# Kernel tuning notes

Measured on AMD Instinct MI355X. Metric: run time of the kernel, lower is better.

Reference implementation:

```python
import jax, jax.numpy as jnp
import numpy as np

H = 1024  # hidden_dim


def setup_inputs() -> dict:
    key = jax.random.key(0)
    ks = jax.random.split(key, 8)
    B, S = 32, 2048
    value = jax.random.normal(ks[0], (B, S, 2 * H), dtype=jnp.float32)
    query = jax.random.normal(ks[1], (B, 2 * H), dtype=jnp.float32)
    padding_mask = jnp.zeros((B, S), dtype=bool)
    pre_coverage = jax.random.uniform(ks[2], (B, S), dtype=jnp.float32)
    sc = 1.0 / np.sqrt(2 * H)
    Wv = jax.random.normal(ks[3], (2 * H, H), dtype=jnp.float32) * sc  # value_layer.weight^T
    Wq = jax.random.normal(ks[4], (2 * H, H), dtype=jnp.float32) * sc  # query_layer.weight^T
    We = jax.random.normal(ks[5], (H,), dtype=jnp.float32) * (1.0 / np.sqrt(H))  # energy_layer
    Wc = jax.random.normal(ks[6], (H,), dtype=jnp.float32)  # coverage_layer (Linear(1,H))
    return {"value": value, "query": query, "padding_mask": padding_mask,
            "pre_coverage": pre_coverage, "Wv": Wv, "Wq": Wq, "We": We, "Wc": Wc}


def reference(value, query, padding_mask, pre_coverage, Wv, Wq, We, Wc):
    # value: [B,S,2H], query: [B,2H], padding_mask: [B,S] bool, pre_coverage: [B,S]
    v = jnp.einsum('bsf,fh->bsh', value, Wv)          # projected values [B,S,H]
    q = (query @ Wq)[:, None, :]                       # [B,1,H]
    feat = q + v + pre_coverage[:, :, None] * Wc       # coverage term: Linear(1,H)
    scores = jnp.tanh(feat) @ We                       # [B,S]
    scores = jnp.where(padding_mask, -jnp.inf, scores)
    alphas = jax.nn.softmax(scores, axis=-1)           # [B,S]
    context = jnp.einsum('bs,bsh->bh', alphas, v)[:, None, :]  # [B,1,H]
    new_coverage = pre_coverage + alphas
    return context, alphas, new_coverage
```

## Files before the change

### kernel.cpp

```cpp
#include <hip/hip_runtime.h>
#include <hip/hip_bf16.h>

#define HD 1024
#define K2 2048
#define BATCH 32
#define SEQ 2048
#define M_TOT (BATCH * SEQ)

typedef __attribute__((ext_vector_type(4))) float f32x4;
typedef __attribute__((ext_vector_type(8))) short bf16x8;
typedef __attribute__((ext_vector_type(4))) unsigned short u16x4;
typedef __attribute__((ext_vector_type(8))) unsigned short u16x8;

__device__ __forceinline__ float bf2f(unsigned short u) {
    unsigned int x = ((unsigned int)u) << 16;
    return __builtin_bit_cast(float, x);
}
__device__ __forceinline__ unsigned short f2bf(float f) {
    unsigned int x = __builtin_bit_cast(unsigned int, f);
    unsigned int lsb = (x >> 16) & 1u;
    x += 0x7fffu + lsb;
    return (unsigned short)(x >> 16);
}

__device__ __forceinline__ void load_lds_16B(const void* g, void* lds) {
    __builtin_amdgcn_global_load_lds(
        (const __attribute__((address_space(1))) unsigned int*)g,
        (__attribute__((address_space(3))) unsigned int*)lds,
        16, 0, 0);
}

__global__ __launch_bounds__(256) void cvt_value_kernel(
        const float* __restrict__ A, unsigned short* __restrict__ Abf) {
    const size_t stride = (size_t)2048 * 256 * 8;
    size_t i = ((size_t)blockIdx.x * 256 + threadIdx.x) * 8;
    const size_t n = (size_t)M_TOT * K2;
    for (; i < n; i += stride) {
        f32x4 a = *reinterpret_cast<const f32x4*>(A + i);
        f32x4 b = *reinterpret_cast<const f32x4*>(A + i + 4);
        u16x8 r;
        r[0] = f2bf(a.x); r[1] = f2bf(a.y); r[2] = f2bf(a.z); r[3] = f2bf(a.w);
        r[4] = f2bf(b.x); r[5] = f2bf(b.y); r[6] = f2bf(b.z); r[7] = f2bf(b.w);
        *reinterpret_cast<u16x8*>(Abf + i) = r;
    }
}

__global__ __launch_bounds__(256) void wv_transpose_kernel(
        const float* __restrict__ Wv, unsigned short* __restrict__ WvT) {
    __shared__ float t[64][65];
    int n0 = blockIdx.x * 64;
    int k0 = blockIdx.y * 64;
    int tx = threadIdx.x & 63, ty = threadIdx.x >> 6;
#pragma unroll
    for (int rr = 0; rr < 16; ++rr) {
        int row = ty + rr * 4;
        t[row][tx] = Wv[(size_t)(k0 + row) * HD + n0 + tx];
    }
    __syncthreads();
#pragma unroll
    for (int rr = 0; rr < 16; ++rr) {
        int row = ty + rr * 4;
        WvT[(size_t)(n0 + row) * K2 + k0 + tx] = f2bf(t[tx][row]);
    }
}

__global__ __launch_bounds__(256) void qproj_kernel(
        const float* __restrict__ query, const float* __restrict__ Wq,
        float* __restrict__ qp) {
    int b = blockIdx.x >> 2;
    int h = ((blockIdx.x & 3) << 8) + threadIdx.x;
    const float* q = query + (size_t)b * K2;
    float acc = 0.f;
    for (int f = 0; f < K2; f += 4) {
        f32x4 qv = *reinterpret_cast<const f32x4*>(q + f);
        acc += qv.x * Wq[(size_t)f * HD + h];
        acc += qv.y * Wq[(size_t)(f + 1) * HD + h];
        acc += qv.z * Wq[(size_t)(f + 2) * HD + h];
        acc += qv.w * Wq[(size_t)(f + 3) * HD + h];
    }
    qp[b * HD + h] = acc;
}

#define NT 32

__device__ __forceinline__ f32x4 mfma_bf16(bf16x8 a, bf16x8 b, f32x4 c) {
    return __builtin_amdgcn_mfma_f32_16x16x32_bf16(a, b, c, 0, 0, 0);
}

template<int MB, int NB>
__device__ __forceinline__ void mfma_quad(f32x4 (&acc)[8][4],
        const bf16x8 (&af)[4][2], const bf16x8 (&bfv)[2][2]) {
#pragma unroll
    for (int f = 0; f < 4; ++f)
#pragma unroll
        for (int j = 0; j < 2; ++j) {
            acc[MB + f][NB + j] = mfma_bf16(af[f][0], bfv[j][0], acc[MB + f][NB + j]);
            acc[MB + f][NB + j] = mfma_bf16(af[f][1], bfv[j][1], acc[MB + f][NB + j]);
        }
}

__global__ __launch_bounds__(512, 2) void gemm8_kernel(
        const unsigned short* __restrict__ A,
        const unsigned short* __restrict__ BT,
        unsigned short* __restrict__ Vout) {
    __shared__ __align__(16) char lds[131072];

    const int tid  = threadIdx.x;
    const int lane = tid & 63;
    const int wave = tid >> 6;
    const int wr   = wave >> 2;
    const int wc   = wave & 3;

    int id  = blockIdx.x;
    int xcd = id & 7, sdx = id >> 3;
    int m0 = ((xcd << 5) | (sdx >> 2)) * 256;
    int n0 = (sdx & 3) * 256;

    const int off0   = wave * 1024 + lane * 16;
    const int srow   = off0 >> 7;
    const int schunk = ((off0 >> 4) & 7) ^ (srow & 7);
    const int scol   = schunk * 8;
    const unsigned short* As0 = A  + ((size_t)m0 + srow) * K2 + scol;
    const unsigned short* Bs0 = BT + ((size_t)n0 + srow) * K2 + scol;

    const int l15 = lane & 15, l4v = lane >> 4;
    const int kch0 = (l4v ^ (lane & 7)) << 4;
    const int kch1 = ((4 | l4v) ^ (lane & 7)) << 4;
    const int aRow = (wr * 128 + l15) * 128;
    const int bRow = (wc * 64 + l15) * 128;

    f32x4 acc[8][4] = {};

#define STG_A(t_, h_, p_, buf_) \
    load_lds_16B(As0 + ((size_t)((h_) * 128 + (p_) * 64)) * K2 + (t_) * 64, \
                 lds + (buf_) * 32768 + (h_) * 16384 + (p_) * 8192 + off0)
#define STG_B(t_, h_, p_, buf_) \
    load_lds_16B(Bs0 + ((size_t)((h_) * 128 + (p_) * 64)) * K2 + (t_) * 64, \
                 lds + 65536 + (buf_) * 32768 + (h_) * 16384 + (p_) * 8192 + off0)

    STG_A(0, 0, 0, 0); STG_A(0, 0, 1, 0); STG_A(0, 1, 0, 0); STG_A(0, 1, 1, 0);
    STG_B(0, 0, 0, 0); STG_B(0, 0, 1, 0); STG_B(0, 1, 0, 0); STG_B(0, 1, 1, 0);
    STG_A(1, 0, 0, 1); STG_A(1, 0, 1, 1); STG_A(1, 1, 0, 1); STG_A(1, 1, 1, 1);
    STG_B(1, 0, 0, 1); STG_B(1, 0, 1, 1); STG_B(1, 1, 0, 1); STG_B(1, 1, 1, 1);
    asm volatile("s_waitcnt vmcnt(8)" ::: "memory");
    __builtin_amdgcn_s_barrier();

    bf16x8 afr[4][2], bf0[2][2], bf1[2][2];

    for (int t = 0; t < NT; ++t) {
        const int cur = t & 1;
        const char* La = lds + cur * 32768;
        const char* Lb = lds + 65536 + cur * 32768;
        const bool pf = (t + 2 < NT);

#pragma unroll
        for (int f = 0; f < 4; ++f) {
            afr[f][0] = *(const bf16x8*)(La + aRow + f * 2048 + kch0);
            afr[f][1] = *(const bf16x8*)(La + aRow + f * 2048 + kch1);
        }
#pragma unroll
        for (int j = 0; j < 2; ++j) {
            bf0[j][0] = *(const bf16x8*)(Lb + bRow + j * 2048 + kch0);
            bf0[j][1] = *(const bf16x8*)(Lb + bRow + j * 2048 + kch1);
        }
        __builtin_amdgcn_s_barrier();
        asm volatile("s_waitcnt lgkmcnt(0)" ::: "memory");
        __builtin_amdgcn_s_setprio(1);
        mfma_quad<0, 0>(acc, afr, bf0);
        __builtin_amdgcn_s_setprio(0);
        __builtin_amdgcn_s_barrier();

#pragma unroll
        for (int j = 0; j < 2; ++j) {
            bf1[j][0] = *(const bf16x8*)(Lb + bRow + (2 + j) * 2048 + kch0);
            bf1[j][1] = *(const bf16x8*)(Lb + bRow + (2 + j) * 2048 + kch1);
        }
        if (pf) { STG_A(t + 2, 0, 0, cur); STG_A(t + 2, 1, 0, cur); }
        __builtin_amdgcn_s_barrier();
        asm volatile("s_waitcnt lgkmcnt(0)" ::: "memory");
        __builtin_amdgcn_s_setprio(1);
        mfma_quad<0, 2>(acc, afr, bf1);
        __builtin_amdgcn_s_setprio(0);
        __builtin_amdgcn_s_barrier();

#pragma unroll
        for (int f = 0; f < 4; ++f) {
            afr[f][0] = *(const bf16x8*)(La + aRow + 8192 + f * 2048 + kch0);
            afr[f][1] = *(const bf16x8*)(La + aRow + 8192 + f * 2048 + kch1);
        }
        if (pf) {
            STG_B(t + 2, 0, 0, cur); STG_B(t + 2, 0, 1, cur);
            STG_B(t + 2, 1, 0, cur); STG_B(t + 2, 1, 1, cur);
        }
        __builtin_amdgcn_s_barrier();
        asm volatile("s_waitcnt lgkmcnt(0)" ::: "memory");
        __builtin_amdgcn_s_setprio(1);
        mfma_quad<4, 2>(acc, afr, bf1);
        __builtin_amdgcn_s_setprio(0);
        __builtin_amdgcn_s_barrier();

        if (pf) { STG_A(t + 2, 0, 1, cur); STG_A(t + 2, 1, 1, cur); }
        __builtin_amdgcn_s_barrier();
        __builtin_amdgcn_s_setprio(1);
        mfma_quad<4, 0>(acc, afr, bf0);
        __builtin_amdgcn_s_setprio(0);
        if (t < NT - 1) {
            if (t < NT - 2) asm volatile("s_waitcnt vmcnt(8)" ::: "memory");
            else            asm volatile("s_waitcnt vmcnt(0)" ::: "memory");
            __builtin_amdgcn_s_barrier();
        }
    }
#undef STG_A
#undef STG_B

#pragma unroll
    for (int fi = 0; fi < 8; ++fi) {
#pragma unroll
        for (int fj = 0; fj < 4; ++fj) {
            int row = m0 + wr * 128 + fi * 16 + l4v * 4;
            int col = n0 + wc * 64 + fj * 16 + l15;
#pragma unroll
            for (int r = 0; r < 4; ++r)
                Vout[(size_t)(row + r) * HD + col] = f2bf(acc[fi][fj][r]);
        }
    }
}

#define BM 128
#define BN 128
#define BK 32
__device__ __forceinline__ void swizzle_mn(int id, int& m0, int& n0) {
    int xcd = id & 7;
    int s = id >> 3;
    int m_idx = (xcd << 6) | (s >> 3);
    int n_idx = s & 7;
    m0 = m_idx * BM;
    n0 = n_idx * BN;
}

__global__ __launch_bounds__(256) void gemm_v_kernel(
        const float* __restrict__ A,
        const unsigned short* __restrict__ BT,
        unsigned short* __restrict__ Vout) {
    __shared__ __align__(16) unsigned short As[BM * BK];
    __shared__ __align__(16) unsigned short Bs[BN * BK];
    const int tid = threadIdx.x;
    const int lane = tid & 63;
    const int wave = tid >> 6;
    const int wr = wave >> 1, wc = wave & 1;
    int m0, n0;
    swizzle_mn(blockIdx.x, m0, n0);
    const int l15 = lane & 15;
    const int l4 = lane >> 4;

    f32x4 acc[4][4] = {};

    for (int kk = 0; kk < K2; kk += BK) {
#pragma unroll
        for (int i = 0; i < 4; ++i) {
            int c = i * 256 + tid;
            int row = c >> 3;
            int col = (c & 7) * 4;
            f32x4 v = *reinterpret_cast<const f32x4*>(
                A + (size_t)(m0 + row) * K2 + kk + col);
            u16x4 bv;
            bv.x = f2bf(v.x); bv.y = f2bf(v.y);
            bv.z = f2bf(v.z); bv.w = f2bf(v.w);
            *reinterpret_cast<u16x4*>(&As[row * BK + col]) = bv;
        }
#pragma unroll
        for (int i = 0; i < 2; ++i) {
            int cb = i * 256 + tid;
            int row = cb >> 2, col = (cb & 3) * 8;
            load_lds_16B(BT + (size_t)(n0 + row) * K2 + kk + col, ((char*)Bs) + cb * 16);
        }
        __syncthreads();

        bf16x8 af[4], bfr[4];
#pragma unroll
        for (int i = 0; i < 4; ++i) {
            int row = wr * 64 + i * 16 + l15;
            af[i] = *reinterpret_cast<const bf16x8*>(&As[row * BK + l4 * 8]);
        }
#pragma unroll
        for (int j = 0; j < 4; ++j) {
            int row = wc * 64 + j * 16 + l15;
            bfr[j] = *reinterpret_cast<const bf16x8*>(&Bs[row * BK + l4 * 8]);
        }
#pragma unroll
        for (int i = 0; i < 4; ++i)
#pragma unroll
            for (int j = 0; j < 4; ++j)
                acc[i][j] = __builtin_amdgcn_mfma_f32_16x16x32_bf16(
                    af[i], bfr[j], acc[i][j], 0, 0, 0);
        __syncthreads();
    }

#pragma unroll
    for (int i = 0; i < 4; ++i) {
#pragma unroll
        for (int j = 0; j < 4; ++j) {
            int row = m0 + wr * 64 + i * 16 + l4 * 4;
            int col = n0 + wc * 64 + j * 16 + l15;
#pragma unroll
            for (int r = 0; r < 4; ++r)
                Vout[(size_t)(row + r) * HD + col] = f2bf(acc[i][j][r]);
        }
    }
}

__global__ __launch_bounds__(256) void score_kernel(
        const unsigned short* __restrict__ V, const float* __restrict__ qp,
        const float* __restrict__ Wc, const float* __restrict__ We,
        const float* __restrict__ pre_cov, float* __restrict__ scores) {
    int lane = threadIdx.x & 63;
    int wave = threadIdx.x >> 6;
    int m = blockIdx.x * 4 + wave;
    int b = m >> 11;
    float pc = pre_cov[m];
    const unsigned short* vp = V + (size_t)m * HD;
    const float* qpb = qp + b * HD;
    float partial = 0.f;
#pragma unroll
    for (int e = 0; e < 16; ++e) {
        int h = e * 64 + lane;
        float f = bf2f(vp[h]) + qpb[h] + pc * Wc[h];
        float t = 1.f - 2.f / (__expf(2.f * f) + 1.f);
        partial += t * We[h];
    }
#pragma unroll
    for (int off = 32; off; off >>= 1)
        partial += __shfl_xor(partial, off);
    if (lane == 0) scores[m] = partial;
}

__global__ __launch_bounds__(256) void softmax_kernel(
        const float* __restrict__ scores, const unsigned char* __restrict__ mask,
        const float* __restrict__ pre_cov, float* __restrict__ out) {
    __shared__ float red[8];
    int b = blockIdx.x;
    int tid = threadIdx.x;
    int lane = tid & 63, wave = tid >> 6;
    float s[8];
#pragma unroll
    for (int i = 0; i < 8; ++i) {
        int idx = b * SEQ + i * 256 + tid;
        float v = scores[idx];
        if (mask[idx]) v = -INFINITY;
        s[i] = v;
    }
    float mx = s[0];
#pragma unroll
    for (int i = 1; i < 8; ++i) mx = fmaxf(mx, s[i]);
#pragma unroll
    for (int off = 32; off; off >>= 1) mx = fmaxf(mx, __shfl_xor(mx, off));
    if (lane == 0) red[wave] = mx;
    __syncthreads();
    mx = fmaxf(fmaxf(red[0], red[1]), fmaxf(red[2], red[3]));

    float e[8]; float sum = 0.f;
#pragma unroll
    for (int i = 0; i < 8; ++i) { e[i] = __expf(s[i] - mx); sum += e[i]; }
#pragma unroll
    for (int off = 32; off; off >>= 1) sum += __shfl_xor(sum, off);
    if (lane == 0) red[4 + wave] = sum;
    __syncthreads();
    sum = red[4] + red[5] + red[6] + red[7];
    float inv = 1.f / sum;
#pragma unroll
    for (int i = 0; i < 8; ++i) {
        int idx = b * SEQ + i * 256 + tid;
        float a = e[i] * inv;
        out[32768 + idx] = a;
        out[32768 + 65536 + idx] = pre_cov[idx] + a;
    }
}

__global__ __launch_bounds__(256) void ctx_part_kernel(
        const unsigned short* __restrict__ V, const float* __restrict__ out,
        float* __restrict__ part) {
    int blk = blockIdx.x;
    int hc = blk & 3;
    int sc = (blk >> 2) & 15;
    int b  = blk >> 6;
    int h = hc * 256 + threadIdx.x;
    const float* al = out + 32768 + b * SEQ + sc * 128;
    const unsigned short* vp = V + ((size_t)(b * SEQ + sc * 128)) * HD + h;
    float acc = 0.f;
#pragma unroll 8
    for (int s = 0; s < 128; ++s)
        acc += al[s] * bf2f(vp[(size_t)s * HD]);
    part[(size_t)(b * 16 + sc) * HD + h] = acc;
}

__global__ __launch_bounds__(256) void ctx_reduce_kernel(
        const float* __restrict__ part, float* __restrict__ out) {
    int idx = blockIdx.x * 256 + threadIdx.x;
    int b = idx >> 10, h = idx & 1023;
    float acc = 0.f;
#pragma unroll
    for (int sc = 0; sc < 16; ++sc)
        acc += part[(size_t)(b * 16 + sc) * HD + h];
    out[idx] = acc;
}

extern "C" void kernel_launch(void* const* d_in, const int* in_sizes, int n_in,
                              void* d_out, int out_size, void* d_ws, size_t ws_size,
                              hipStream_t stream) {
    const float* value          = (const float*)d_in[0];
    const float* query          = (const float*)d_in[1];
    const unsigned char* mask   = (const unsigned char*)d_in[2];
    const float* pre_cov        = (const float*)d_in[3];
    const float* Wv             = (const float*)d_in[4];
    const float* Wq             = (const float*)d_in[5];
    const float* We             = (const float*)d_in[6];
    const float* Wc             = (const float*)d_in[7];
    float* out = (float*)d_out;

    char* ws = (char*)d_ws;
    unsigned short* WvT = (unsigned short*)(ws);
    unsigned short* Vbf = (unsigned short*)(ws + ((size_t)4 << 20));
    float* qp           = (float*)(ws + ((size_t)132 << 20));
    float* scores       = (float*)(ws + ((size_t)132 << 20) + (128 << 10));
    float* part         = (float*)(ws + ((size_t)132 << 20) + (384 << 10));
    unsigned short* Abf = (unsigned short*)(ws + ((size_t)136 << 20));

    const bool bigws = ws_size >= ((size_t)392 << 20);

    hipLaunchKernelGGL(wv_transpose_kernel, dim3(16, 32), dim3(256), 0, stream, Wv, WvT);
    hipLaunchKernelGGL(qproj_kernel, dim3(128), dim3(256), 0, stream, query, Wq, qp);
    if (bigws) {
        hipLaunchKernelGGL(cvt_value_kernel, dim3(2048), dim3(256), 0, stream, value, Abf);
        hipLaunchKernelGGL(gemm8_kernel, dim3(1024), dim3(512), 0, stream, Abf, WvT, Vbf);
    } else {
        hipLaunchKernelGGL(gemm_v_kernel, dim3(4096), dim3(256), 0, stream, value, WvT, Vbf);
    }
    hipLaunchKernelGGL(score_kernel, dim3(M_TOT / 4), dim3(256), 0, stream,
                       Vbf, qp, Wc, We, pre_cov, scores);
    hipLaunchKernelGGL(softmax_kernel, dim3(BATCH), dim3(256), 0, stream,
                       scores, mask, pre_cov, out);
    hipLaunchKernelGGL(ctx_part_kernel, dim3(2048), dim3(256), 0, stream, Vbf, out, part);
    hipLaunchKernelGGL(ctx_reduce_kernel, dim3(128), dim3(256), 0, stream, part, out);
}
```

Baseline: 521.8 us.

## Fuse fp32-to-bf16 value conversion into GEMM A-tile staging; vectorize context partials

Drops the separate cvt_value kernel. The GEMM now loads fp32 value rows into registers, converts them with packed bf16 conversion instructions and writes the swizzled tiles to LDS itself, which avoids writing and re-reading a 256MB bf16 copy of value. A loads for tile t+2 are issued during tile t and written to LDS in later phases, replacing direct global-to-LDS loads. This costs more registers and VALU work and changes the waitcnt scheme. The context partial kernel now has each thread handle 4 hidden columns with vector loads, launching a quarter as many blocks.

```diff
diff --git a/kernel.cpp b/kernel.cpp
--- a/kernel.cpp
+++ b/kernel.cpp
@@ -11,6 +11,7 @@
 typedef __attribute__((ext_vector_type(8))) short bf16x8;
 typedef __attribute__((ext_vector_type(4))) unsigned short u16x4;
 typedef __attribute__((ext_vector_type(8))) unsigned short u16x8;
+typedef __attribute__((ext_vector_type(4))) unsigned int u32x4;
 
 __device__ __forceinline__ float bf2f(unsigned short u) {
     unsigned int x = ((unsigned int)u) << 16;
@@ -22,27 +23,17 @@
     x += 0x7fffu + lsb;
     return (unsigned short)(x >> 16);
 }
+__device__ __forceinline__ unsigned int cvt_pk(float lo, float hi) {
+    unsigned int r;
+    asm("v_cvt_pk_bf16_f32 %0, %1, %2" : "=v"(r) : "v"(lo), "v"(hi));
+    return r;
+}
 
 __device__ __forceinline__ void load_lds_16B(const void* g, void* lds) {
     __builtin_amdgcn_global_load_lds(
         (const __attribute__((address_space(1))) unsigned int*)g,
         (__attribute__((address_space(3))) unsigned int*)lds,
         16, 0, 0);
-}
-
-__global__ __launch_bounds__(256) void cvt_value_kernel(
-        const float* __restrict__ A, unsigned short* __restrict__ Abf) {
-    const size_t stride = (size_t)2048 * 256 * 8;
-    size_t i = ((size_t)blockIdx.x * 256 + threadIdx.x) * 8;
-    const size_t n = (size_t)M_TOT * K2;
-    for (; i < n; i += stride) {
-        f32x4 a = *reinterpret_cast<const f32x4*>(A + i);
-        f32x4 b = *reinterpret_cast<const f32x4*>(A + i + 4);
-        u16x8 r;
-        r[0] = f2bf(a.x); r[1] = f2bf(a.y); r[2] = f2bf(a.z); r[3] = f2bf(a.w);
-        r[4] = f2bf(b.x); r[5] = f2bf(b.y); r[6] = f2bf(b.z); r[7] = f2bf(b.w);
-        *reinterpret_cast<u16x8*>(Abf + i) = r;
-    }
 }
 
 __global__ __launch_bounds__(256) void wv_transpose_kernel(
@@ -100,7 +91,7 @@
 }
 
 __global__ __launch_bounds__(512, 2) void gemm8_kernel(
-        const unsigned short* __restrict__ A,
+        const float* __restrict__ A,
         const unsigned short* __restrict__ BT,
         unsigned short* __restrict__ Vout) {
     __shared__ __align__(16) char lds[131072];
@@ -118,10 +109,11 @@
 
     const int off0   = wave * 1024 + lane * 16;
     const int srow   = off0 >> 7;
-    const int schunk = ((off0 >> 4) & 7) ^ (srow & 7);
-    const int scol   = schunk * 8;
-    const unsigned short* As0 = A  + ((size_t)m0 + srow) * K2 + scol;
-    const unsigned short* Bs0 = BT + ((size_t)n0 + srow) * K2 + scol;
+    const int chunk  = (off0 >> 4) & 7;
+    const int schunk = chunk ^ (srow & 7);
+    const unsigned short* Bs0 = BT + ((size_t)n0 + srow) * K2 + schunk * 8;
+    const float* aBase = A + ((size_t)m0 + srow) * K2 + chunk * 8;
+    const int woff = srow * 128 + schunk * 16;
 
     const int l15 = lane & 15, l4v = lane >> 4;
     const int kch0 = (l4v ^ (lane & 7)) << 4;
@@ -131,18 +123,51 @@
 
     f32x4 acc[8][4] = {};
 
-#define STG_A(t_, h_, p_, buf_) \
-    load_lds_16B(As0 + ((size_t)((h_) * 128 + (p_) * 64)) * K2 + (t_) * 64, \
-                 lds + (buf_) * 32768 + (h_) * 16384 + (p_) * 8192 + off0)
+    f32x4 a0lo, a0hi, a1lo, a1hi, a2lo, a2hi, a3lo, a3hi;
+
+#define LOAD_A(t_) do {                                                       \
+        const float* _ap = aBase + (size_t)(t_) * 64;                         \
+        a0lo = *(const f32x4*)(_ap);                                          \
+        a0hi = *(const f32x4*)(_ap + 4);                                      \
+        a1lo = *(const f32x4*)(_ap + (size_t)128 * K2);                       \
+        a1hi = *(const f32x4*)(_ap + (size_t)128 * K2 + 4);                   \
+        a2lo = *(const f32x4*)(_ap + (size_t)64 * K2);                        \
+        a2hi = *(const f32x4*)(_ap + (size_t)64 * K2 + 4);                    \
+        a3lo = *(const f32x4*)(_ap + (size_t)192 * K2);                       \
+        a3hi = *(const f32x4*)(_ap + (size_t)192 * K2 + 4);                   \
+    } while (0)
+
+#define WRITE_A_P0(buf_) do {                                                 \
+        u32x4 w0, w1;                                                         \
+        w0.x = cvt_pk(a0lo.x, a0lo.y); w0.y = cvt_pk(a0lo.z, a0lo.w);         \
+        w0.z = cvt_pk(a0hi.x, a0hi.y); w0.w = cvt_pk(a0hi.z, a0hi.w);         \
+        w1.x = cvt_pk(a1lo.x, a1lo.y); w1.y = cvt_pk(a1lo.z, a1lo.w);         \
+        w1.z = cvt_pk(a1hi.x, a1hi.y); w1.w = cvt_pk(a1hi.z, a1hi.w);         \
+        *reinterpret_cast<u32x4*>(lds + (buf_) * 32768 + 0     + woff) = w0;  \
+        *reinterpret_cast<u32x4*>(lds + (buf_) * 32768 + 16384 + woff) = w1;  \
+    } while (0)
+
+#define WRITE_A_P1(buf_) do {                                                 \
+        u32x4 w2, w3;                                                         \
+        w2.x = cvt_pk(a2lo.x, a2lo.y); w2.y = cvt_pk(a2lo.z, a2lo.w);         \
+        w2.z = cvt_pk(a2hi.x, a2hi.y); w2.w = cvt_pk(a2hi.z, a2hi.w);         \
+        w3.x = cvt_pk(a3lo.x, a3lo.y); w3.y = cvt_pk(a3lo.z, a3lo.w);         \
+        w3.z = cvt_pk(a3hi.x, a3hi.y); w3.w = cvt_pk(a3hi.z, a3hi.w);         \
+        *reinterpret_cast<u32x4*>(lds + (buf_) * 32768 + 8192  + woff) = w2;  \
+        *reinterpret_cast<u32x4*>(lds + (buf_) * 32768 + 24576 + woff) = w3;  \
+    } while (0)
+
 #define STG_B(t_, h_, p_, buf_) \
     load_lds_16B(Bs0 + ((size_t)((h_) * 128 + (p_) * 64)) * K2 + (t_) * 64, \
                  lds + 65536 + (buf_) * 32768 + (h_) * 16384 + (p_) * 8192 + off0)
 
-    STG_A(0, 0, 0, 0); STG_A(0, 0, 1, 0); STG_A(0, 1, 0, 0); STG_A(0, 1, 1, 0);
+    LOAD_A(0);
     STG_B(0, 0, 0, 0); STG_B(0, 0, 1, 0); STG_B(0, 1, 0, 0); STG_B(0, 1, 1, 0);
-    STG_A(1, 0, 0, 1); STG_A(1, 0, 1, 1); STG_A(1, 1, 0, 1); STG_A(1, 1, 1, 1);
+    WRITE_A_P0(0); WRITE_A_P1(0);
+    LOAD_A(1);
     STG_B(1, 0, 0, 1); STG_B(1, 0, 1, 1); STG_B(1, 1, 0, 1); STG_B(1, 1, 1, 1);
-    asm volatile("s_waitcnt vmcnt(8)" ::: "memory");
+    WRITE_A_P0(1); WRITE_A_P1(1);
+    asm volatile("s_waitcnt vmcnt(0) lgkmcnt(0)" ::: "memory");
     __builtin_amdgcn_s_barrier();
 
     bf16x8 afr[4][2], bf0[2][2], bf1[2][2];
@@ -163,6 +188,7 @@
             bf0[j][0] = *(const bf16x8*)(Lb + bRow + j * 2048 + kch0);
             bf0[j][1] = *(const bf16x8*)(Lb + bRow + j * 2048 + kch1);
         }
+        if (pf) LOAD_A(t + 2);
         __builtin_amdgcn_s_barrier();
         asm volatile("s_waitcnt lgkmcnt(0)" ::: "memory");
         __builtin_amdgcn_s_setprio(1);
@@ -175,7 +201,6 @@
             bf1[j][0] = *(const bf16x8*)(Lb + bRow + (2 + j) * 2048 + kch0);
             bf1[j][1] = *(const bf16x8*)(Lb + bRow + (2 + j) * 2048 + kch1);
         }
-        if (pf) { STG_A(t + 2, 0, 0, cur); STG_A(t + 2, 1, 0, cur); }
         __builtin_amdgcn_s_barrier();
         asm volatile("s_waitcnt lgkmcnt(0)" ::: "memory");
         __builtin_amdgcn_s_setprio(1);
@@ -189,6 +214,7 @@
             afr[f][1] = *(const bf16x8*)(La + aRow + 8192 + f * 2048 + kch1);
         }
         if (pf) {
+            WRITE_A_P0(cur);
             STG_B(t + 2, 0, 0, cur); STG_B(t + 2, 0, 1, cur);
             STG_B(t + 2, 1, 0, cur); STG_B(t + 2, 1, 1, cur);
         }
@@ -199,18 +225,18 @@
         __builtin_amdgcn_s_setprio(0);
         __builtin_amdgcn_s_barrier();
 
-        if (pf) { STG_A(t + 2, 0, 1, cur); STG_A(t + 2, 1, 1, cur); }
-        __builtin_amdgcn_s_barrier();
+        if (pf) WRITE_A_P1(cur);
+        __builtin_amdgcn_s_barrier();
+        asm volatile("s_waitcnt lgkmcnt(0)" ::: "memory");
         __builtin_amdgcn_s_setprio(1);
         mfma_quad<4, 0>(acc, afr, bf0);
         __builtin_amdgcn_s_setprio(0);
-        if (t < NT - 1) {
-            if (t < NT - 2) asm volatile("s_waitcnt vmcnt(8)" ::: "memory");
-            else            asm volatile("s_waitcnt vmcnt(0)" ::: "memory");
-            __builtin_amdgcn_s_barrier();
-        }
-    }
-#undef STG_A
+        if (t == NT - 2) asm volatile("s_waitcnt vmcnt(0)" ::: "memory");
+        if (t < NT - 1) __builtin_amdgcn_s_barrier();
+    }
+#undef LOAD_A
+#undef WRITE_A_P0
+#undef WRITE_A_P1
 #undef STG_B
 
 #pragma unroll
@@ -380,17 +406,22 @@
         const unsigned short* __restrict__ V, const float* __restrict__ out,
         float* __restrict__ part) {
     int blk = blockIdx.x;
-    int hc = blk & 3;
-    int sc = (blk >> 2) & 15;
-    int b  = blk >> 6;
-    int h = hc * 256 + threadIdx.x;
+    int sc = blk & 15;
+    int b  = blk >> 4;
+    int h4 = threadIdx.x * 4;
     const float* al = out + 32768 + b * SEQ + sc * 128;
-    const unsigned short* vp = V + ((size_t)(b * SEQ + sc * 128)) * HD + h;
-    float acc = 0.f;
-#pragma unroll 8
-    for (int s = 0; s < 128; ++s)
-        acc += al[s] * bf2f(vp[(size_t)s * HD]);
-    part[(size_t)(b * 16 + sc) * HD + h] = acc;
+    const unsigned short* vp = V + ((size_t)(b * SEQ + sc * 128)) * HD + h4;
+    f32x4 acc = {};
+#pragma unroll 4
+    for (int s = 0; s < 128; ++s) {
+        float a = al[s];
+        u16x4 v = *reinterpret_cast<const u16x4*>(vp + (size_t)s * HD);
+        acc.x += a * bf2f(v.x);
+        acc.y += a * bf2f(v.y);
+        acc.z += a * bf2f(v.z);
+        acc.w += a * bf2f(v.w);
+    }
+    *reinterpret_cast<f32x4*>(&part[(size_t)(b * 16 + sc) * HD + h4]) = acc;
 }
 
 __global__ __launch_bounds__(256) void ctx_reduce_kernel(
@@ -423,15 +454,13 @@
     float* qp           = (float*)(ws + ((size_t)132 << 20));
     float* scores       = (float*)(ws + ((size_t)132 << 20) + (128 << 10));
     float* part         = (float*)(ws + ((size_t)132 << 20) + (384 << 10));
-    unsigned short* Abf = (unsigned short*)(ws + ((size_t)136 << 20));
-
-    const bool bigws = ws_size >= ((size_t)392 << 20);
+
+    const bool bigws = ws_size >= ((size_t)136 << 20);
 
     hipLaunchKernelGGL(wv_transpose_kernel, dim3(16, 32), dim3(256), 0, stream, Wv, WvT);
     hipLaunchKernelGGL(qproj_kernel, dim3(128), dim3(256), 0, stream, query, Wq, qp);
     if (bigws) {
-        hipLaunchKernelGGL(cvt_value_kernel, dim3(2048), dim3(256), 0, stream, value, Abf);
-        hipLaunchKernelGGL(gemm8_kernel, dim3(1024), dim3(512), 0, stream, Abf, WvT, Vbf);
+        hipLaunchKernelGGL(gemm8_kernel, dim3(1024), dim3(512), 0, stream, value, WvT, Vbf);
     } else {
         hipLaunchKernelGGL(gemm_v_kernel, dim3(4096), dim3(256), 0, stream, value, WvT, Vbf);
     }
@@ -439,6 +468,6 @@
                        Vbf, qp, Wc, We, pre_cov, scores);
     hipLaunchKernelGGL(softmax_kernel, dim3(BATCH), dim3(256), 0, stream,
                        scores, mask, pre_cov, out);
-    hipLaunchKernelGGL(ctx_part_kernel, dim3(2048), dim3(256), 0, stream, Vbf, out, part);
+    hipLaunchKernelGGL(ctx_part_kernel, dim3(512), dim3(256), 0, stream, Vbf, out, part);
     hipLaunchKernelGGL(ctx_reduce_kernel, dim3(128), dim3(256), 0, stream, part, out);
 }
```

Measured after the change: 504.0 us. 1.04x faster.

## Chunk value conversion and GEMM by rows; vectorize context partial sums

Applied to the files above, without the earlier changes.

Splits the fp32-to-bf16 conversion and the bf16 GEMM into four row chunks of 16384 rows, each converted and then immediately multiplied. The aim is for each chunk's bf16 data (64 MB) to still be cache-resident when the GEMM reads it, instead of streaming the full 256 MB through HBM twice. The context partial kernel now uses 4-wide vector loads and accumulators per thread with a quarter of the blocks. In exchange there are more launches and fewer GEMM blocks per launch (256), which may leave CUs underused at chunk boundaries.

```diff
diff --git a/kernel.cpp b/kernel.cpp
--- a/kernel.cpp
+++ b/kernel.cpp
@@ -6,6 +6,7 @@
 #define BATCH 32
 #define SEQ 2048
 #define M_TOT (BATCH * SEQ)
+#define MCHUNK 16384
 
 typedef __attribute__((ext_vector_type(4))) float f32x4;
 typedef __attribute__((ext_vector_type(8))) short bf16x8;
@@ -32,9 +33,9 @@
 
 __global__ __launch_bounds__(256) void cvt_value_kernel(
         const float* __restrict__ A, unsigned short* __restrict__ Abf) {
-    const size_t stride = (size_t)2048 * 256 * 8;
+    const size_t stride = (size_t)512 * 256 * 8;
     size_t i = ((size_t)blockIdx.x * 256 + threadIdx.x) * 8;
-    const size_t n = (size_t)M_TOT * K2;
+    const size_t n = (size_t)MCHUNK * K2;
     for (; i < n; i += stride) {
         f32x4 a = *reinterpret_cast<const f32x4*>(A + i);
         f32x4 b = *reinterpret_cast<const f32x4*>(A + i + 4);
@@ -102,7 +103,8 @@
 __global__ __launch_bounds__(512, 2) void gemm8_kernel(
         const unsigned short* __restrict__ A,
         const unsigned short* __restrict__ BT,
-        unsigned short* __restrict__ Vout) {
+        unsigned short* __restrict__ Vout,
+        int m_base) {
     __shared__ __align__(16) char lds[131072];
 
     const int tid  = threadIdx.x;
@@ -113,7 +115,7 @@
 
     int id  = blockIdx.x;
     int xcd = id & 7, sdx = id >> 3;
-    int m0 = ((xcd << 5) | (sdx >> 2)) * 256;
+    int m0 = m_base + ((xcd << 3) | (sdx >> 2)) * 256;
     int n0 = (sdx & 3) * 256;
 
     const int off0   = wave * 1024 + lane * 16;
@@ -380,17 +382,22 @@
         const unsigned short* __restrict__ V, const float* __restrict__ out,
         float* __restrict__ part) {
     int blk = blockIdx.x;
-    int hc = blk & 3;
-    int sc = (blk >> 2) & 15;
-    int b  = blk >> 6;
-    int h = hc * 256 + threadIdx.x;
+    int sc = blk & 15;
+    int b  = blk >> 4;
+    int h4 = threadIdx.x * 4;
     const float* al = out + 32768 + b * SEQ + sc * 128;
-    const unsigned short* vp = V + ((size_t)(b * SEQ + sc * 128)) * HD + h;
-    float acc = 0.f;
-#pragma unroll 8
-    for (int s = 0; s < 128; ++s)
-        acc += al[s] * bf2f(vp[(size_t)s * HD]);
-    part[(size_t)(b * 16 + sc) * HD + h] = acc;
+    const unsigned short* vp = V + ((size_t)(b * SEQ + sc * 128)) * HD + h4;
+    f32x4 acc = {};
+#pragma unroll 4
+    for (int s = 0; s < 128; ++s) {
+        float a = al[s];
+        u16x4 v = *reinterpret_cast<const u16x4*>(vp + (size_t)s * HD);
+        acc.x += a * bf2f(v.x);
+        acc.y += a * bf2f(v.y);
+        acc.z += a * bf2f(v.z);
+        acc.w += a * bf2f(v.w);
+    }
+    *reinterpret_cast<f32x4*>(&part[(size_t)(b * 16 + sc) * HD + h4]) = acc;
 }
 
 __global__ __launch_bounds__(256) void ctx_reduce_kernel(
@@ -430,8 +437,13 @@
     hipLaunchKernelGGL(wv_transpose_kernel, dim3(16, 32), dim3(256), 0, stream, Wv, WvT);
     hipLaunchKernelGGL(qproj_kernel, dim3(128), dim3(256), 0, stream, query, Wq, qp);
     if (bigws) {
-        hipLaunchKernelGGL(cvt_value_kernel, dim3(2048), dim3(256), 0, stream, value, Abf);
-        hipLaunchKernelGGL(gemm8_kernel, dim3(1024), dim3(512), 0, stream, Abf, WvT, Vbf);
+        for (int c = 0; c < 4; ++c) {
+            const size_t eoff = (size_t)c * MCHUNK * K2;
+            hipLaunchKernelGGL(cvt_value_kernel, dim3(512), dim3(256), 0, stream,
+                               value + eoff, Abf + eoff);
+            hipLaunchKernelGGL(gemm8_kernel, dim3(256), dim3(512), 0, stream,
+                               Abf, WvT, Vbf, c * MCHUNK);
+        }
     } else {
         hipLaunchKernelGGL(gemm_v_kernel, dim3(4096), dim3(256), 0, stream, value, WvT, Vbf);
     }
@@ -439,6 +451,6 @@
                        Vbf, qp, Wc, We, pre_cov, scores);
     hipLaunchKernelGGL(softmax_kernel, dim3(BATCH), dim3(256), 0, stream,
                        scores, mask, pre_cov, out);
-    hipLaunchKernelGGL(ctx_part_kernel, dim3(2048), dim3(256), 0, stream, Vbf, out, part);
+    hipLaunchKernelGGL(ctx_part_kernel, dim3(512), dim3(256), 0, stream, Vbf, out, part);
     hipLaunchKernelGGL(ctx_reduce_kernel, dim3(128), dim3(256), 0, stream, part, out);
 }
```

Result: no change. 524.7 us (+0.6%).
